# Optimization experiments

Measured on AMD Instinct MI355X. Metric: run time of the kernel, lower is better.

## Reference

```python
import jax, jax.numpy as jnp
import numpy as np

N, D, E, R, G, M = 8192, 1024, 64, 64, 8, 8

def setup_inputs() -> dict:
    key = jax.random.key(0)
    k_h, k_wg, k_wl, k_w1, k_w2 = jax.random.split(key, 5)
    return {
        'h': jax.random.normal(k_h, (N, D), jnp.float32),
        'Wg': jax.random.normal(k_wg, (D, G), jnp.float32) * 0.02,  # nn.Linear weight (transposed)
        'bg': jnp.zeros((G,), jnp.float32),
        'Wloc': jax.random.normal(k_wl, (G, D, M), jnp.float32) * 0.02,
        'W1': jax.random.normal(k_w1, (E, D, R), jnp.float32) * 0.02,
        'W2': jax.random.normal(k_w2, (E, R, D), jnp.float32) * 0.02,
        'k': 2,
    }

def reference(h, Wg, bg, Wloc, W1, W2, k):
    n, d = h.shape
    g, _, m = Wloc.shape
    e = W1.shape[0]
    router_temp = 1.0
    # stage 1: group routing (top-1)
    g_scores = h @ Wg + bg                                   # (N, G)
    group_idx = jnp.argmax(g_scores, axis=-1)                # (N,)
    # stage 2: within-group scores; compute all groups (cheap: N*G*M) then select
    all_local = jnp.einsum('nd,gdm->ngm', h, Wloc)           # (N, G, M)
    local_scores = jnp.take_along_axis(all_local, group_idx[:, None, None], axis=1)[:, 0]  # (N, M)
    topv, topm = jax.lax.top_k(local_scores, k)              # (N, k)
    gate = jax.nn.softmax(topv / max(router_temp, 1e-6), axis=-1)
    expert_ids = group_idx[:, None] * m + topm               # (N, k) global expert ids
    # scatter gates into dense (N, E); topm entries are distinct per token
    gate_full = jnp.zeros((n, e), h.dtype).at[jnp.arange(n)[:, None], expert_ids].set(gate)
    # low-rank expert compute: relu(h @ W1) @ W2, weighted-combined
    tmp = jax.nn.relu(jnp.einsum('nd,edr->ner', h, W1))      # (N, E, R)
    out = jnp.einsum('ner,erd->nd', gate_full[:, :, None] * tmp, W2)  # (N, D)
    return out, expert_ids, gate, group_idx
```

## Files before the change

kernel.cpp:

```cpp
#include <hip/hip_runtime.h>
#include <hip/hip_bf16.h>
#include <cstdint>
#include <cstddef>

#define NTOK 8192
#define DIM  1024
#define NEXP 64
#define RANK 64
#define NGRP 8
#define NLOC 8
#define ECAP 2048

typedef __attribute__((ext_vector_type(8))) short bf16x8;
typedef __attribute__((ext_vector_type(4))) float f32x4;

static __device__ inline unsigned int pack_bf16x2(float a, float b) {
    __hip_bfloat16 ha = __float2bfloat16(a);
    __hip_bfloat16 hb = __float2bfloat16(b);
    return (unsigned int)(*(unsigned short*)&ha) |
           ((unsigned int)(*(unsigned short*)&hb) << 16);
}

__global__ __launch_bounds__(512) void score_all(
    const float* __restrict__ h, const float* __restrict__ Wt,
    unsigned short* __restrict__ hb, float* __restrict__ Sp)
{
    __shared__ float Hs[128][66];

    const int tile = blockIdx.x;
    const int slab = blockIdx.y;
    const int z    = blockIdx.z;
    const int tid  = threadIdx.x;
    const int wave = tid >> 6;
    const int lane = tid & 63;
    const int t0   = tile * 128;
    const int kz   = z * 512;

    const int r0  = tid >> 2;
    const int seg = (tid & 3) * 16;

    const int c0g = slab ? (40 + wave * 4) : (wave * 5);
    const float* wt0 = Wt + (size_t)c0g * 1024;

    float acc[10] = {};

    float4 hpre[4];
    {
        const float* src = h + (size_t)(t0 + r0) * DIM + kz + seg;
        hpre[0] = *(const float4*)(src);
        hpre[1] = *(const float4*)(src + 4);
        hpre[2] = *(const float4*)(src + 8);
        hpre[3] = *(const float4*)(src + 12);
    }

    for (int chunk = 0; chunk < 8; ++chunk) {
        const int kb = kz + chunk * 64;

        {
            float* dst = &Hs[r0][seg];
#pragma unroll
            for (int q = 0; q < 4; ++q) {
                const float4 v = hpre[q];
                *(float2*)(dst + q * 4)     = make_float2(v.x, v.y);
                *(float2*)(dst + q * 4 + 2) = make_float2(v.z, v.w);
            }
            if (slab == 0) {
                unsigned short* hrow = hb + (size_t)(t0 + r0) * DIM + kb + seg;
#pragma unroll
                for (int q = 0; q < 4; ++q) {
                    const float4 v = hpre[q];
                    uint2 pk;
                    pk.x = pack_bf16x2(v.x, v.y);
                    pk.y = pack_bf16x2(v.z, v.w);
                    *(uint2*)(hrow + q * 4) = pk;
                }
            }
        }
        __syncthreads();

        if (chunk < 7) {
            const float* src = h + (size_t)(t0 + r0) * DIM + kb + 64 + seg;
            hpre[0] = *(const float4*)(src);
            hpre[1] = *(const float4*)(src + 4);
            hpre[2] = *(const float4*)(src + 8);
            hpre[3] = *(const float4*)(src + 12);
        }

        if (slab == 0) {
#pragma unroll 4
            for (int kq = 0; kq < 16; ++kq) {
                const int k0 = kq * 4;
                const float* wtk = wt0 + kb + k0;
                float4 bq[5];
#pragma unroll
                for (int c = 0; c < 5; ++c)
                    bq[c] = *(const float4*)(wtk + (size_t)c * 1024);
                const float2 a00 = *(const float2*)&Hs[lane][k0];
                const float2 a01 = *(const float2*)&Hs[lane][k0 + 2];
                const float2 a10 = *(const float2*)&Hs[64 + lane][k0];
                const float2 a11 = *(const float2*)&Hs[64 + lane][k0 + 2];
#pragma unroll
                for (int c = 0; c < 5; ++c) {
                    acc[c] += a00.x * bq[c].x; acc[5 + c] += a10.x * bq[c].x;
                }
#pragma unroll
                for (int c = 0; c < 5; ++c) {
                    acc[c] += a00.y * bq[c].y; acc[5 + c] += a10.y * bq[c].y;
                }
#pragma unroll
                for (int c = 0; c < 5; ++c) {
                    acc[c] += a01.x * bq[c].z; acc[5 + c] += a11.x * bq[c].z;
                }
#pragma unroll
                for (int c = 0; c < 5; ++c) {
                    acc[c] += a01.y * bq[c].w; acc[5 + c] += a11.y * bq[c].w;
                }
            }
        } else {
#pragma unroll 4
            for (int kq = 0; kq < 16; ++kq) {
                const int k0 = kq * 4;
                const float* wtk = wt0 + kb + k0;
                float4 bq[4];
#pragma unroll
                for (int c = 0; c < 4; ++c)
                    bq[c] = *(const float4*)(wtk + (size_t)c * 1024);
                const float2 a00 = *(const float2*)&Hs[lane][k0];
                const float2 a01 = *(const float2*)&Hs[lane][k0 + 2];
                const float2 a10 = *(const float2*)&Hs[64 + lane][k0];
                const float2 a11 = *(const float2*)&Hs[64 + lane][k0 + 2];
#pragma unroll
                for (int c = 0; c < 4; ++c) {
                    acc[c] += a00.x * bq[c].x; acc[5 + c] += a10.x * bq[c].x;
                }
#pragma unroll
                for (int c = 0; c < 4; ++c) {
                    acc[c] += a00.y * bq[c].y; acc[5 + c] += a10.y * bq[c].y;
                }
#pragma unroll
                for (int c = 0; c < 4; ++c) {
                    acc[c] += a01.x * bq[c].z; acc[5 + c] += a11.x * bq[c].z;
                }
#pragma unroll
                for (int c = 0; c < 4; ++c) {
                    acc[c] += a01.y * bq[c].w; acc[5 + c] += a11.y * bq[c].w;
                }
            }
        }
        __syncthreads();
    }

    const int nout = slab ? 4 : 5;
    float* dstS  = Sp + (size_t)z * (NTOK * 72) + (size_t)(t0 + lane) * 72 + c0g;
    float* dstS2 = Sp + (size_t)z * (NTOK * 72) + (size_t)(t0 + 64 + lane) * 72 + c0g;
#pragma unroll
    for (int c = 0; c < 5; ++c) {
        if (c < nout) {
            dstS[c]  = acc[c];
            dstS2[c] = acc[5 + c];
        }
    }
}

__global__ __launch_bounds__(256) void route_all(
    const float* __restrict__ Sp, const float* __restrict__ bg,
    float* __restrict__ out_gidx, float* __restrict__ out_eid,
    float* __restrict__ out_gate, int* __restrict__ cursor,
    int* __restrict__ token_list, float* __restrict__ slot_gate)
{
    const int t = blockIdx.x * 256 + threadIdx.x;
    const float* p0 = Sp + (size_t)t * 72;
    const float* p1 = p0 + (size_t)NTOK * 72;
    float s[72];
#pragma unroll
    for (int i = 0; i < 18; ++i) {
        const float4 a = *(const float4*)(p0 + i * 4);
        const float4 b = *(const float4*)(p1 + i * 4);
        s[i * 4 + 0] = a.x + b.x; s[i * 4 + 1] = a.y + b.y;
        s[i * 4 + 2] = a.z + b.z; s[i * 4 + 3] = a.w + b.w;
    }

    int gi = 0; float best = s[0] + bg[0];
#pragma unroll
    for (int g = 1; g < NGRP; ++g) {
        const float v = s[g] + bg[g];
        if (v > best) { best = v; gi = g; }
    }

    float ls[NLOC];
#pragma unroll
    for (int m = 0; m < NLOC; ++m) ls[m] = s[8 + gi * NLOC + m];

    int m1 = 0; float v1 = ls[0];
#pragma unroll
    for (int m = 1; m < NLOC; ++m) { if (ls[m] > v1) { v1 = ls[m]; m1 = m; } }
    int m2 = (m1 == 0) ? 1 : 0; float v2 = ls[m2];
#pragma unroll
    for (int m = 0; m < NLOC; ++m) {
        if (m != m1 && m != ((m1 == 0) ? 1 : 0) && ls[m] > v2) { v2 = ls[m]; m2 = m; }
    }
    const float e2v = expf(v2 - v1);
    const float inv = 1.f / (1.f + e2v);
    const float g0 = inv, g1 = e2v * inv;
    const int ea = gi * NLOC + m1, eb = gi * NLOC + m2;

    out_gidx[t] = (float)gi;
    out_eid[t * 2 + 0] = (float)ea;
    out_eid[t * 2 + 1] = (float)eb;
    out_gate[t * 2 + 0] = g0;
    out_gate[t * 2 + 1] = g1;

    const int pA = atomicAdd(&cursor[ea], 1);
    if (pA < ECAP) {
        token_list[ea * ECAP + pA] = t * 2 + 0;
        slot_gate[ea * ECAP + pA] = g0;
    }
    const int pB = atomicAdd(&cursor[eb], 1);
    if (pB < ECAP) {
        token_list[eb * ECAP + pB] = t * 2 + 1;
        slot_gate[eb * ECAP + pB] = g1;
    }
}

__global__ __launch_bounds__(256) void prep_w(
    const float* __restrict__ W1, const float* __restrict__ W2,
    const float* __restrict__ Wg, const float* __restrict__ Wloc,
    unsigned short* __restrict__ W1t, unsigned short* __restrict__ W2t,
    float* __restrict__ Wt)
{
    __shared__ float Ls[64][65];
    const int e = blockIdx.x;
    const int y = blockIdx.y;
    if (y == 32) {
        if (e < 36) {
#pragma unroll
            for (int cc = 0; cc < 2; ++cc) {
                const int c = e * 2 + cc;
                const float* src = (c < 8)
                    ? (Wg + c)
                    : (Wloc + (size_t)((c - 8) >> 3) * (DIM * NLOC) + ((c - 8) & 7));
                for (int k = threadIdx.x; k < DIM; k += 256)
                    Wt[(size_t)c * DIM + k] = src[(size_t)k * NLOC];
            }
        }
        return;
    }
    if (y < 16) {
        const int kb = y;
        const float* src = W1 + (size_t)e * DIM * RANK + (size_t)kb * 64 * RANK;
#pragma unroll
        for (int it = 0; it < 4; ++it) {
            const int kk = (threadIdx.x >> 4) + it * 16;
            const int rr = (threadIdx.x & 15) * 4;
            *(float4*)&Ls[kk][rr] = *(const float4*)(src + (size_t)kk * RANK + rr);
        }
        __syncthreads();
#pragma unroll
        for (int it = 0; it < 2; ++it) {
            const int idx = threadIdx.x + it * 256;
            const int r = idx >> 3, k8 = (idx & 7) * 8;
            uint4 v;
            v.x = pack_bf16x2(Ls[k8 + 0][r], Ls[k8 + 1][r]);
            v.y = pack_bf16x2(Ls[k8 + 2][r], Ls[k8 + 3][r]);
            v.z = pack_bf16x2(Ls[k8 + 4][r], Ls[k8 + 5][r]);
            v.w = pack_bf16x2(Ls[k8 + 6][r], Ls[k8 + 7][r]);
            *(uint4*)(W1t + (size_t)e * RANK * DIM + (size_t)r * DIM + kb * 64 + k8) = v;
        }
    } else {
        const int db = y - 16;
        const float* src = W2 + (size_t)e * RANK * DIM + db * 64;
#pragma unroll
        for (int it = 0; it < 4; ++it) {
            const int rr = (threadIdx.x >> 4) + it * 16;
            const int dd = (threadIdx.x & 15) * 4;
            *(float4*)&Ls[rr][dd] = *(const float4*)(src + (size_t)rr * DIM + dd);
        }
        __syncthreads();
#pragma unroll
        for (int it = 0; it < 2; ++it) {
            const int idx = threadIdx.x + it * 256;
            const int d = idx >> 3, r8 = (idx & 7) * 8;
            uint4 v;
            v.x = pack_bf16x2(Ls[r8 + 0][d], Ls[r8 + 1][d]);
            v.y = pack_bf16x2(Ls[r8 + 2][d], Ls[r8 + 3][d]);
            v.z = pack_bf16x2(Ls[r8 + 4][d], Ls[r8 + 5][d]);
            v.w = pack_bf16x2(Ls[r8 + 6][d], Ls[r8 + 7][d]);
            *(uint4*)(W2t + (size_t)e * DIM * RANK + (size_t)(db * 64 + d) * RANK + r8) = v;
        }
    }
}

__global__ __launch_bounds__(256, 2) void e1_mfma(
    const unsigned short* __restrict__ hb, const unsigned short* __restrict__ W1t,
    const int* __restrict__ counts, const int* __restrict__ token_list,
    const float* __restrict__ slot_gate, unsigned short* __restrict__ P)
{
    __shared__ unsigned short Hs[64 * 72];
    __shared__ unsigned short Ws[64 * 72];
    __shared__ int   tokS[64];
    __shared__ float gateS[64];

    const int e   = blockIdx.x;
    const int tid = threadIdx.x;
    const int ne  = min(counts[e], ECAP);
    const int base = e * ECAP;

    const unsigned short* W1te = W1t + (size_t)e * RANK * DIM;
    const int wave = tid >> 6;
    const int lane = tid & 63;
    const int tx   = lane & 15;
    const int quad = lane >> 4;

    for (int tile = blockIdx.y; tile * 64 < ne; tile += 8) {
        const int row0 = tile * 64;
        __syncthreads();
        if (tid < 64) {
            const int gr = row0 + tid;
            tokS[tid]  = (gr < ne) ? token_list[base + gr] : -1;
            gateS[tid] = (gr < ne) ? slot_gate[base + gr] : 0.f;
        }
        f32x4 acc[4] = {};
        for (int kc = 0; kc < DIM; kc += 64) {
            __syncthreads();
#pragma unroll
            for (int it = 0; it < 2; ++it) {
                const int idx = tid + it * 256;
                const int s = idx >> 3, k8 = (idx & 7) * 8;
                const int ent = tokS[s];
                uint4 v = make_uint4(0, 0, 0, 0);
                if (ent >= 0)
                    v = *(const uint4*)(hb + (size_t)(ent >> 1) * DIM + kc + k8);
                *(uint4*)(Hs + s * 72 + k8) = v;
            }
#pragma unroll
            for (int it = 0; it < 2; ++it) {
                const int idx = tid + it * 256;
                const int r = idx >> 3, k8 = (idx & 7) * 8;
                *(uint4*)(Ws + r * 72 + k8) =
                    *(const uint4*)(W1te + (size_t)r * DIM + kc + k8);
            }
            __syncthreads();
#pragma unroll
            for (int ks = 0; ks < 2; ++ks) {
                const bf16x8 a = *(const bf16x8*)(Hs + (wave * 16 + tx) * 72 + ks * 32 + quad * 8);
#pragma unroll
                for (int j = 0; j < 4; ++j) {
                    const bf16x8 b = *(const bf16x8*)(Ws + (j * 16 + tx) * 72 + ks * 32 + quad * 8);
                    acc[j] = __builtin_amdgcn_mfma_f32_16x16x32_bf16(a, b, acc[j], 0, 0, 0);
                }
            }
        }
#pragma unroll
        for (int j = 0; j < 4; ++j) {
#pragma unroll
            for (int i = 0; i < 4; ++i) {
                const int sl = wave * 16 + quad * 4 + i;
                const int gr = row0 + sl;
                if (gr < ne) {
                    const float v = fmaxf(acc[j][i], 0.f) * gateS[sl];
                    __hip_bfloat16 hv = __float2bfloat16(v);
                    P[(size_t)(base + gr) * RANK + j * 16 + tx] = *(unsigned short*)&hv;
                }
            }
        }
    }
}

__global__ __launch_bounds__(256, 2) void e2_mfma(
    const unsigned short* __restrict__ P, const unsigned short* __restrict__ W2t,
    const int* __restrict__ counts, const int* __restrict__ token_list,
    float* __restrict__ out, float* __restrict__ contrib)
{
    __shared__ unsigned short Ps[64 * 72];
    __shared__ unsigned short W2s[64 * 72];
    __shared__ int tokS[64];

    const int e = blockIdx.x;
    const int colbase = blockIdx.y * 64;
    const int tid = threadIdx.x;
    const int ne  = min(counts[e], ECAP);
    const int base = e * ECAP;

    const unsigned short* W2te = W2t + (size_t)e * DIM * RANK;
    const int wave = tid >> 6;
    const int lane = tid & 63;
    const int tx   = lane & 15;
    const int quad = lane >> 4;

#pragma unroll
    for (int it = 0; it < 2; ++it) {
        const int idx = tid + it * 256;
        const int d = idx >> 3, r8 = (idx & 7) * 8;
        *(uint4*)(W2s + d * 72 + r8) =
            *(const uint4*)(W2te + (size_t)(colbase + d) * RANK + r8);
    }

    for (int tile = blockIdx.z; tile * 64 < ne; tile += 4) {
        const int row0 = tile * 64;
        __syncthreads();
        if (tid < 64) {
            const int gr = row0 + tid;
            tokS[tid] = (gr < ne) ? token_list[base + gr] : -1;
        }
#pragma unroll
        for (int it = 0; it < 2; ++it) {
            const int idx = tid + it * 256;
            const int s = idx >> 3, r8 = (idx & 7) * 8;
            const int gr = row0 + s;
            uint4 v = make_uint4(0, 0, 0, 0);
            if (gr < ne) v = *(const uint4*)(P + (size_t)(base + gr) * RANK + r8);
            *(uint4*)(Ps + s * 72 + r8) = v;
        }
        __syncthreads();
        f32x4 acc[4] = {};
#pragma unroll
        for (int ks = 0; ks < 2; ++ks) {
            const bf16x8 a = *(const bf16x8*)(Ps + (wave * 16 + tx) * 72 + ks * 32 + quad * 8);
#pragma unroll
            for (int j = 0; j < 4; ++j) {
                const bf16x8 b = *(const bf16x8*)(W2s + (j * 16 + tx) * 72 + ks * 32 + quad * 8);
                acc[j] = __builtin_amdgcn_mfma_f32_16x16x32_bf16(a, b, acc[j], 0, 0, 0);
            }
        }
#pragma unroll
        for (int i = 0; i < 4; ++i) {
            const int sl = wave * 16 + quad * 4 + i;
            const int ent = tokS[sl];
            if (ent >= 0) {
                float* basep = (ent & 1) ? contrib : out;
                float* op = basep + (size_t)(ent >> 1) * DIM + colbase;
#pragma unroll
                for (int j = 0; j < 4; ++j)
                    op[j * 16 + tx] = acc[j][i];
            }
        }
    }
}

__global__ __launch_bounds__(256) void combine_kernel(
    const float* __restrict__ contrib, float* __restrict__ out)
{
    const size_t i = (size_t)blockIdx.x * 256 + threadIdx.x;
    float4 a = ((const float4*)out)[i];
    const float4 b = ((const float4*)contrib)[i];
    a.x += b.x; a.y += b.y; a.z += b.z; a.w += b.w;
    ((float4*)out)[i] = a;
}

extern "C" void kernel_launch(void* const* d_in, const int* in_sizes, int n_in,
                              void* d_out, int out_size, void* d_ws, size_t ws_size,
                              hipStream_t stream)
{
    const float* h    = (const float*)d_in[0];
    const float* Wg   = (const float*)d_in[1];
    const float* bg   = (const float*)d_in[2];
    const float* Wloc = (const float*)d_in[3];
    const float* W1   = (const float*)d_in[4];
    const float* W2   = (const float*)d_in[5];

    float* out_f    = (float*)d_out;
    float* out_main = out_f;
    float* out_eid  = out_f + (size_t)NTOK * DIM;
    float* out_gate = out_eid + (size_t)NTOK * 2;
    float* out_gidx = out_gate + (size_t)NTOK * 2;

    int* ws_i        = (int*)d_ws;
    int* cursor_e    = ws_i;
    int* token_list  = ws_i + 1024;
    float* slot_gate = (float*)(ws_i + 1024 + NEXP * ECAP);
    float* Sp        = slot_gate + NEXP * ECAP;
    float* Wt        = Sp + (size_t)2 * NTOK * 72;
    unsigned short* P_h = (unsigned short*)(Wt + 72 * DIM);
    unsigned short* W1t = P_h + (size_t)NEXP * ECAP * RANK;
    unsigned short* W2t = W1t + (size_t)NEXP * RANK * DIM;
    float* contrib      = (float*)(W2t + (size_t)NEXP * DIM * RANK);
    unsigned short* hb = (unsigned short*)contrib;

    hipMemsetAsync(cursor_e, 0, 64 * sizeof(int), stream);

    prep_w<<<dim3(NEXP, 33), 256, 0, stream>>>(W1, W2, Wg, Wloc, W1t, W2t, Wt);
    score_all<<<dim3(64, 2, 2), 512, 0, stream>>>(h, Wt, hb, Sp);
    route_all<<<NTOK / 256, 256, 0, stream>>>(Sp, bg, out_gidx, out_eid,
        out_gate, cursor_e, token_list, slot_gate);
    e1_mfma<<<dim3(NEXP, 8), 256, 0, stream>>>(hb, W1t, cursor_e, token_list,
        slot_gate, P_h);
    e2_mfma<<<dim3(NEXP, 16, 4), 256, 0, stream>>>(P_h, W2t, cursor_e, token_list,
        out_main, contrib);
    combine_kernel<<<(NTOK * DIM / 4) / 256, 256, 0, stream>>>(contrib, out_main);
}
```

Baseline: 266.5 us.

## Fuse expert up/down projections and stage router weights in shared memory

The two expert GEMM kernels are merged into one, so the relu-gated low-rank activations stay in shared memory as bf16 instead of going through a global P buffer. The kernel then loops over all 16 output column blocks per token tile. The score kernel now reads Wg and Wloc directly and stages them transposed into shared memory each chunk, which removes the prep pass that built a transposed weight copy. Trade-offs: the fused grid has fewer blocks (64x8 instead of 64x16x4 for the second stage), so it exposes less parallelism, and W2 is reloaded per tile.

```diff
diff --git a/kernel.cpp b/kernel.cpp
--- a/kernel.cpp
+++ b/kernel.cpp
@@ -22,10 +22,12 @@
 }
 
 __global__ __launch_bounds__(512) void score_all(
-    const float* __restrict__ h, const float* __restrict__ Wt,
-    unsigned short* __restrict__ hb, float* __restrict__ Sp)
+    const float* __restrict__ h, const float* __restrict__ Wg,
+    const float* __restrict__ Wloc, unsigned short* __restrict__ hb,
+    float* __restrict__ Sp)
 {
     __shared__ float Hs[128][66];
+    __shared__ float Ws[40][72];
 
     const int tile = blockIdx.x;
     const int slab = blockIdx.y;
@@ -39,18 +41,29 @@
     const int r0  = tid >> 2;
     const int seg = (tid & 3) * 16;
 
-    const int c0g = slab ? (40 + wave * 4) : (wave * 5);
-    const float* wt0 = Wt + (size_t)c0g * 1024;
-
     float acc[10] = {};
 
     float4 hpre[4];
+    float4 wgp;
+    float4 wlp;
+
     {
-        const float* src = h + (size_t)(t0 + r0) * DIM + kz + seg;
+        const int kb = kz;
+        const float* src = h + (size_t)(t0 + r0) * DIM + kb + seg;
         hpre[0] = *(const float4*)(src);
         hpre[1] = *(const float4*)(src + 4);
         hpre[2] = *(const float4*)(src + 8);
         hpre[3] = *(const float4*)(src + 12);
+        const int g = tid >> 7, r = tid & 127;
+        if (slab == 0) {
+            if (tid < 128)
+                wgp = *(const float4*)(Wg + (size_t)(kb + (tid >> 1)) * NGRP + (tid & 1) * 4);
+            wlp = *(const float4*)(Wloc + (size_t)g * (DIM * NLOC)
+                                       + (size_t)(kb + (r >> 1)) * NLOC + (r & 1) * 4);
+        } else {
+            wlp = *(const float4*)(Wloc + (size_t)(4 + g) * (DIM * NLOC)
+                                       + (size_t)(kb + (r >> 1)) * NLOC + (r & 1) * 4);
+        }
     }
 
     for (int chunk = 0; chunk < 8; ++chunk) {
@@ -76,29 +89,58 @@
                 }
             }
         }
+        {
+            const int g = tid >> 7, r = tid & 127;
+            const int k = r >> 1;
+            if (slab == 0) {
+                if (tid < 128) {
+                    const int kk = tid >> 1, m4 = (tid & 1) * 4;
+                    Ws[m4 + 0][kk] = wgp.x; Ws[m4 + 1][kk] = wgp.y;
+                    Ws[m4 + 2][kk] = wgp.z; Ws[m4 + 3][kk] = wgp.w;
+                }
+                const int c = 8 + g * 8 + (r & 1) * 4;
+                Ws[c + 0][k] = wlp.x; Ws[c + 1][k] = wlp.y;
+                Ws[c + 2][k] = wlp.z; Ws[c + 3][k] = wlp.w;
+            } else {
+                const int c = g * 8 + (r & 1) * 4;
+                Ws[c + 0][k] = wlp.x; Ws[c + 1][k] = wlp.y;
+                Ws[c + 2][k] = wlp.z; Ws[c + 3][k] = wlp.w;
+            }
+        }
         __syncthreads();
 
         if (chunk < 7) {
-            const float* src = h + (size_t)(t0 + r0) * DIM + kb + 64 + seg;
+            const int kbn = kb + 64;
+            const float* src = h + (size_t)(t0 + r0) * DIM + kbn + seg;
             hpre[0] = *(const float4*)(src);
             hpre[1] = *(const float4*)(src + 4);
             hpre[2] = *(const float4*)(src + 8);
             hpre[3] = *(const float4*)(src + 12);
+            const int g = tid >> 7, r = tid & 127;
+            if (slab == 0) {
+                if (tid < 128)
+                    wgp = *(const float4*)(Wg + (size_t)(kbn + (tid >> 1)) * NGRP + (tid & 1) * 4);
+                wlp = *(const float4*)(Wloc + (size_t)g * (DIM * NLOC)
+                                           + (size_t)(kbn + (r >> 1)) * NLOC + (r & 1) * 4);
+            } else {
+                wlp = *(const float4*)(Wloc + (size_t)(4 + g) * (DIM * NLOC)
+                                           + (size_t)(kbn + (r >> 1)) * NLOC + (r & 1) * 4);
+            }
         }
 
         if (slab == 0) {
-#pragma unroll 4
+            const int c0 = wave * 5;
+#pragma unroll 2
             for (int kq = 0; kq < 16; ++kq) {
                 const int k0 = kq * 4;
-                const float* wtk = wt0 + kb + k0;
-                float4 bq[5];
-#pragma unroll
-                for (int c = 0; c < 5; ++c)
-                    bq[c] = *(const float4*)(wtk + (size_t)c * 1024);
                 const float2 a00 = *(const float2*)&Hs[lane][k0];
                 const float2 a01 = *(const float2*)&Hs[lane][k0 + 2];
                 const float2 a10 = *(const float2*)&Hs[64 + lane][k0];
                 const float2 a11 = *(const float2*)&Hs[64 + lane][k0 + 2];
+                float4 bq[5];
+#pragma unroll
+                for (int c = 0; c < 5; ++c)
+                    bq[c] = *(const float4*)&Ws[c0 + c][k0];
 #pragma unroll
                 for (int c = 0; c < 5; ++c) {
                     acc[c] += a00.x * bq[c].x; acc[5 + c] += a10.x * bq[c].x;
@@ -117,18 +159,18 @@
                 }
             }
         } else {
-#pragma unroll 4
+            const int c0 = wave * 4;
+#pragma unroll 2
             for (int kq = 0; kq < 16; ++kq) {
                 const int k0 = kq * 4;
-                const float* wtk = wt0 + kb + k0;
-                float4 bq[4];
-#pragma unroll
-                for (int c = 0; c < 4; ++c)
-                    bq[c] = *(const float4*)(wtk + (size_t)c * 1024);
                 const float2 a00 = *(const float2*)&Hs[lane][k0];
                 const float2 a01 = *(const float2*)&Hs[lane][k0 + 2];
                 const float2 a10 = *(const float2*)&Hs[64 + lane][k0];
                 const float2 a11 = *(const float2*)&Hs[64 + lane][k0 + 2];
+                float4 bq[4];
+#pragma unroll
+                for (int c = 0; c < 4; ++c)
+                    bq[c] = *(const float4*)&Ws[c0 + c][k0];
 #pragma unroll
                 for (int c = 0; c < 4; ++c) {
                     acc[c] += a00.x * bq[c].x; acc[5 + c] += a10.x * bq[c].x;
@@ -150,9 +192,10 @@
         __syncthreads();
     }
 
+    const int gcol = (slab ? 40 + wave * 4 : wave * 5);
     const int nout = slab ? 4 : 5;
-    float* dstS  = Sp + (size_t)z * (NTOK * 72) + (size_t)(t0 + lane) * 72 + c0g;
-    float* dstS2 = Sp + (size_t)z * (NTOK * 72) + (size_t)(t0 + 64 + lane) * 72 + c0g;
+    float* dstS  = Sp + (size_t)z * (NTOK * 72) + (size_t)(t0 + lane) * 72 + gcol;
+    float* dstS2 = Sp + (size_t)z * (NTOK * 72) + (size_t)(t0 + 64 + lane) * 72 + gcol;
 #pragma unroll
     for (int c = 0; c < 5; ++c) {
         if (c < nout) {
@@ -224,27 +267,11 @@
 
 __global__ __launch_bounds__(256) void prep_w(
     const float* __restrict__ W1, const float* __restrict__ W2,
-    const float* __restrict__ Wg, const float* __restrict__ Wloc,
-    unsigned short* __restrict__ W1t, unsigned short* __restrict__ W2t,
-    float* __restrict__ Wt)
+    unsigned short* __restrict__ W1t, unsigned short* __restrict__ W2t)
 {
     __shared__ float Ls[64][65];
     const int e = blockIdx.x;
     const int y = blockIdx.y;
-    if (y == 32) {
-        if (e < 36) {
-#pragma unroll
-            for (int cc = 0; cc < 2; ++cc) {
-                const int c = e * 2 + cc;
-                const float* src = (c < 8)
-                    ? (Wg + c)
-                    : (Wloc + (size_t)((c - 8) >> 3) * (DIM * NLOC) + ((c - 8) & 7));
-                for (int k = threadIdx.x; k < DIM; k += 256)
-                    Wt[(size_t)c * DIM + k] = src[(size_t)k * NLOC];
-            }
-        }
-        return;
-    }
     if (y < 16) {
         const int kb = y;
         const float* src = W1 + (size_t)e * DIM * RANK + (size_t)kb * 64 * RANK;
@@ -290,22 +317,26 @@
     }
 }
 
-__global__ __launch_bounds__(256, 2) void e1_mfma(
+__global__ __launch_bounds__(256, 2) void e12_mfma(
     const unsigned short* __restrict__ hb, const unsigned short* __restrict__ W1t,
-    const int* __restrict__ counts, const int* __restrict__ token_list,
-    const float* __restrict__ slot_gate, unsigned short* __restrict__ P)
+    const unsigned short* __restrict__ W2t, const int* __restrict__ counts,
+    const int* __restrict__ token_list, const float* __restrict__ slot_gate,
+    float* __restrict__ out, float* __restrict__ contrib)
 {
     __shared__ unsigned short Hs[64 * 72];
     __shared__ unsigned short Ws[64 * 72];
+    __shared__ unsigned short Ps[64 * 72];
+    __shared__ unsigned short W2s[64 * 72];
     __shared__ int   tokS[64];
     __shared__ float gateS[64];
 
-    const int e   = blockIdx.x;
-    const int tid = threadIdx.x;
-    const int ne  = min(counts[e], ECAP);
+    const int e    = blockIdx.x;
+    const int tid  = threadIdx.x;
+    const int ne   = min(counts[e], ECAP);
     const int base = e * ECAP;
 
     const unsigned short* W1te = W1t + (size_t)e * RANK * DIM;
+    const unsigned short* W2te = W2t + (size_t)e * DIM * RANK;
     const int wave = tid >> 6;
     const int lane = tid & 63;
     const int tx   = lane & 15;
@@ -319,6 +350,7 @@
             tokS[tid]  = (gr < ne) ? token_list[base + gr] : -1;
             gateS[tid] = (gr < ne) ? slot_gate[base + gr] : 0.f;
         }
+
         f32x4 acc[4] = {};
         for (int kc = 0; kc < DIM; kc += 64) {
             __syncthreads();
@@ -350,89 +382,52 @@
                 }
             }
         }
+
 #pragma unroll
         for (int j = 0; j < 4; ++j) {
 #pragma unroll
             for (int i = 0; i < 4; ++i) {
                 const int sl = wave * 16 + quad * 4 + i;
-                const int gr = row0 + sl;
-                if (gr < ne) {
-                    const float v = fmaxf(acc[j][i], 0.f) * gateS[sl];
-                    __hip_bfloat16 hv = __float2bfloat16(v);
-                    P[(size_t)(base + gr) * RANK + j * 16 + tx] = *(unsigned short*)&hv;
-                }
-            }
-        }
-    }
-}
-
-__global__ __launch_bounds__(256, 2) void e2_mfma(
-    const unsigned short* __restrict__ P, const unsigned short* __restrict__ W2t,
-    const int* __restrict__ counts, const int* __restrict__ token_list,
-    float* __restrict__ out, float* __restrict__ contrib)
-{
-    __shared__ unsigned short Ps[64 * 72];
-    __shared__ unsigned short W2s[64 * 72];
-    __shared__ int tokS[64];
-
-    const int e = blockIdx.x;
-    const int colbase = blockIdx.y * 64;
-    const int tid = threadIdx.x;
-    const int ne  = min(counts[e], ECAP);
-    const int base = e * ECAP;
-
-    const unsigned short* W2te = W2t + (size_t)e * DIM * RANK;
-    const int wave = tid >> 6;
-    const int lane = tid & 63;
-    const int tx   = lane & 15;
-    const int quad = lane >> 4;
-
-#pragma unroll
-    for (int it = 0; it < 2; ++it) {
-        const int idx = tid + it * 256;
-        const int d = idx >> 3, r8 = (idx & 7) * 8;
-        *(uint4*)(W2s + d * 72 + r8) =
-            *(const uint4*)(W2te + (size_t)(colbase + d) * RANK + r8);
-    }
-
-    for (int tile = blockIdx.z; tile * 64 < ne; tile += 4) {
-        const int row0 = tile * 64;
-        __syncthreads();
-        if (tid < 64) {
-            const int gr = row0 + tid;
-            tokS[tid] = (gr < ne) ? token_list[base + gr] : -1;
-        }
-#pragma unroll
-        for (int it = 0; it < 2; ++it) {
-            const int idx = tid + it * 256;
-            const int s = idx >> 3, r8 = (idx & 7) * 8;
-            const int gr = row0 + s;
-            uint4 v = make_uint4(0, 0, 0, 0);
-            if (gr < ne) v = *(const uint4*)(P + (size_t)(base + gr) * RANK + r8);
-            *(uint4*)(Ps + s * 72 + r8) = v;
-        }
-        __syncthreads();
-        f32x4 acc[4] = {};
-#pragma unroll
-        for (int ks = 0; ks < 2; ++ks) {
-            const bf16x8 a = *(const bf16x8*)(Ps + (wave * 16 + tx) * 72 + ks * 32 + quad * 8);
-#pragma unroll
-            for (int j = 0; j < 4; ++j) {
-                const bf16x8 b = *(const bf16x8*)(W2s + (j * 16 + tx) * 72 + ks * 32 + quad * 8);
-                acc[j] = __builtin_amdgcn_mfma_f32_16x16x32_bf16(a, b, acc[j], 0, 0, 0);
-            }
-        }
-#pragma unroll
-        for (int i = 0; i < 4; ++i) {
-            const int sl = wave * 16 + quad * 4 + i;
-            const int ent = tokS[sl];
-            if (ent >= 0) {
-                float* basep = (ent & 1) ? contrib : out;
-                float* op = basep + (size_t)(ent >> 1) * DIM + colbase;
-#pragma unroll
-                for (int j = 0; j < 4; ++j)
-                    op[j * 16 + tx] = acc[j][i];
-            }
+                const float v = fmaxf(acc[j][i], 0.f) * gateS[sl];
+                __hip_bfloat16 hv = __float2bfloat16(v);
+                Ps[sl * 72 + j * 16 + tx] = *(unsigned short*)&hv;
+            }
+        }
+        __syncthreads();
+
+        for (int cb = 0; cb < 16; ++cb) {
+            const int colbase = cb * 64;
+#pragma unroll
+            for (int it = 0; it < 2; ++it) {
+                const int idx = tid + it * 256;
+                const int d = idx >> 3, r8 = (idx & 7) * 8;
+                *(uint4*)(W2s + d * 72 + r8) =
+                    *(const uint4*)(W2te + (size_t)(colbase + d) * RANK + r8);
+            }
+            __syncthreads();
+            f32x4 acc2[4] = {};
+#pragma unroll
+            for (int ks = 0; ks < 2; ++ks) {
+                const bf16x8 a = *(const bf16x8*)(Ps + (wave * 16 + tx) * 72 + ks * 32 + quad * 8);
+#pragma unroll
+                for (int j = 0; j < 4; ++j) {
+                    const bf16x8 b = *(const bf16x8*)(W2s + (j * 16 + tx) * 72 + ks * 32 + quad * 8);
+                    acc2[j] = __builtin_amdgcn_mfma_f32_16x16x32_bf16(a, b, acc2[j], 0, 0, 0);
+                }
+            }
+#pragma unroll
+            for (int i = 0; i < 4; ++i) {
+                const int sl = wave * 16 + quad * 4 + i;
+                const int ent = tokS[sl];
+                if (ent >= 0) {
+                    float* basep = (ent & 1) ? contrib : out;
+                    float* op = basep + (size_t)(ent >> 1) * DIM + colbase;
+#pragma unroll
+                    for (int j = 0; j < 4; ++j)
+                        op[j * 16 + tx] = acc2[j][i];
+                }
+            }
+            __syncthreads();
         }
     }
 }
@@ -469,22 +464,18 @@
     int* token_list  = ws_i + 1024;
     float* slot_gate = (float*)(ws_i + 1024 + NEXP * ECAP);
     float* Sp        = slot_gate + NEXP * ECAP;
-    float* Wt        = Sp + (size_t)2 * NTOK * 72;
-    unsigned short* P_h = (unsigned short*)(Wt + 72 * DIM);
-    unsigned short* W1t = P_h + (size_t)NEXP * ECAP * RANK;
+    unsigned short* hb  = (unsigned short*)(Sp + (size_t)2 * NTOK * 72);
+    unsigned short* W1t = hb + (size_t)NTOK * DIM;
     unsigned short* W2t = W1t + (size_t)NEXP * RANK * DIM;
     float* contrib      = (float*)(W2t + (size_t)NEXP * DIM * RANK);
-    unsigned short* hb = (unsigned short*)contrib;
 
     hipMemsetAsync(cursor_e, 0, 64 * sizeof(int), stream);
 
-    prep_w<<<dim3(NEXP, 33), 256, 0, stream>>>(W1, W2, Wg, Wloc, W1t, W2t, Wt);
-    score_all<<<dim3(64, 2, 2), 512, 0, stream>>>(h, Wt, hb, Sp);
+    prep_w<<<dim3(NEXP, 32), 256, 0, stream>>>(W1, W2, W1t, W2t);
+    score_all<<<dim3(64, 2, 2), 512, 0, stream>>>(h, Wg, Wloc, hb, Sp);
     route_all<<<NTOK / 256, 256, 0, stream>>>(Sp, bg, out_gidx, out_eid,
         out_gate, cursor_e, token_list, slot_gate);
-    e1_mfma<<<dim3(NEXP, 8), 256, 0, stream>>>(hb, W1t, cursor_e, token_list,
-        slot_gate, P_h);
-    e2_mfma<<<dim3(NEXP, 16, 4), 256, 0, stream>>>(P_h, W2t, cursor_e, token_list,
-        out_main, contrib);
+    e12_mfma<<<dim3(NEXP, 8), 256, 0, stream>>>(hb, W1t, W2t, cursor_e,
+        token_list, slot_gate, out_main, contrib);
     combine_kernel<<<(NTOK * DIM / 4) / 256, 256, 0, stream>>>(contrib, out_main);
 }
```

Result: faster. 239.2 us (-10.2%).
